# Optimization experiments

Measured on AMD Instinct MI355X. Metric: run time of the kernel, lower is better.

Reference implementation:

```python
import jax, jax.numpy as jnp
import numpy as np

ALPHA = 0.01
BETA = 3e-05
OUT_H, OUT_W = 256, 256
KSIZE, SIGMA = 5, 4.0


def _gaussian_kernel2d(ks=KSIZE, sigma=SIGMA):
    x = jnp.arange(ks, dtype=jnp.float32) - (ks - 1) / 2.0
    g = jnp.exp(-(x * x) / (2.0 * sigma * sigma))
    g = g / g.sum()
    return jnp.outer(g, g)  # [ks, ks]


def _gaussian_blur(maps):
    # maps: [B, H, W]; reflect padding + depthwise 5x5 gaussian (kornia-style GaussianBlur2d)
    k = _gaussian_kernel2d()[None, None]  # [1,1,5,5]
    p = KSIZE // 2
    x = jnp.pad(maps[:, None], ((0, 0), (0, 0), (p, p), (p, p)), mode='reflect')
    y = jax.lax.conv_general_dilated(x, k, (1, 1), 'VALID')
    return y[:, 0]


def _resize_bilinear_align_corners(x, oh, ow):
    # x: [B, h, w] -> [B, oh, ow], torch F.interpolate(mode='bilinear', align_corners=True)
    B, h, w = x.shape
    ys = jnp.linspace(0.0, h - 1.0, oh)
    xs = jnp.linspace(0.0, w - 1.0, ow)
    y0 = jnp.floor(ys).astype(jnp.int32)
    x0 = jnp.floor(xs).astype(jnp.int32)
    y1 = jnp.minimum(y0 + 1, h - 1)
    x1 = jnp.minimum(x0 + 1, w - 1)
    fy = (ys - y0.astype(ys.dtype))[:, None]  # [oh,1]
    fx = (xs - x0.astype(xs.dtype))[None, :]  # [1,ow]
    a = x[:, y0][:, :, x0]
    b = x[:, y0][:, :, x1]
    c = x[:, y1][:, :, x0]
    d = x[:, y1][:, :, x1]
    top = a * (1.0 - fx) + b * fx
    bot = c * (1.0 - fx) + d * fx
    return top * (1.0 - fy) + bot * fy


def setup_inputs() -> dict:
    key = jax.random.key(0)
    k0, k1, k2 = jax.random.split(key, 3)
    B = 256
    return {
        'out0': jax.random.normal(k0, (B, 64, 64), jnp.float32),
        'out1': jax.random.normal(k1, (B, 32, 32), jnp.float32),
        'out2': jax.random.normal(k2, (B, 16, 16), jnp.float32),
    }


def reference(out0, out1, out2):
    outputs = [out0, out1, out2]
    B = out0.shape[0]
    # per-sample max of each scale -> softmax-weighted selection of per-sample weight
    max_vals = jnp.stack([o.reshape(B, -1).max(axis=1) for o in outputs], axis=1)  # [B,3]
    probs = jax.nn.softmax(max_vals, axis=1)
    mask = probs > probs.mean(axis=1, keepdims=True)  # probs > prob_mean
    cnt = mask.sum(axis=1)
    sel_mean = (max_vals * mask).sum(axis=1) / jnp.maximum(cnt, 1)
    total_weights = jnp.where(cnt > 0, jnp.maximum(sel_mean * ALPHA, BETA), BETA)  # [B]
    # multi-scale fusion: bilinear(align_corners=True) upsample to (256,256) and sum
    maps = _resize_bilinear_align_corners(out0, OUT_H, OUT_W)
    maps = maps + _resize_bilinear_align_corners(out1, OUT_H, OUT_W)
    maps = maps + _resize_bilinear_align_corners(out2, OUT_H, OUT_W)
    # gaussian blur then per-sample score. torch takes topk(k=f(total_weights)).values[0],
    # and topk values are sorted descending, so values[0] == max (k / total_weights drop out).
    blurred = _gaussian_blur(maps)
    scores = blurred.reshape(B, -1).max(axis=1)
    del total_weights  # only influenced the (unused) top-k size in the original
    return scores[:, None], maps
```

## Files before the change

kernel.cpp:

```cpp
#include <hip/hip_runtime.h>
#include <math.h>


static constexpr int W  = 256;
static constexpr int QB = 16;

__device__ __forceinline__ int reflect256(int i) {
    if (i < 0) i = -i;
    if (i > 255) i = 510 - i;
    return i;
}

__global__ __launch_bounds__(256, 4) void fused_kernel(
    const float* __restrict__ in0,
    const float* __restrict__ in1,
    const float* __restrict__ in2,
    float* __restrict__ part,
    float* __restrict__ maps)
{
    const int t   = threadIdx.x;
    const int q   = t & 63;
    const int wv  = __builtin_amdgcn_readfirstlane(t >> 6);
    const int bid = blockIdx.x;
    const int b   = bid >> 4;
    const int r0  = (bid & 15) * 16;
    const int rw0 = r0 + wv * 4;
    const int c0  = q * 4;

    const int rlo = max(r0 - 2, 0);
    const int rhi = min(r0 + 17, 255);
    const int y0lo = (rlo * 63) / 255;
    const int y1lo = (rlo * 31) / 255;
    const int y2lo = (rlo * 15) / 255;
    const int y0hi = min((rhi * 63) / 255 + 1, 63);
    const int y1hi = min((rhi * 31) / 255 + 1, 31);
    const int y2hi = min((rhi * 15) / 255 + 1, 15);
    const int n0 = y0hi - y0lo + 1;
    const int n1 = y1hi - y1lo + 1;
    const int n2 = y2hi - y2lo + 1;

    __shared__ float lds[4768];
    float* const s0r = lds;
    float* const s1r = lds + 448;
    float* const s2r = lds + 608;
    float* const xr0 = lds + 672;
    float* const xr1 = lds + 2464;
    float* const xr2 = lds + 3744;

    {
        const float4* g0 = (const float4*)(in0 + (size_t)b * 4096 + y0lo * 64);
        const float4* g1 = (const float4*)(in1 + (size_t)b * 1024 + y1lo * 32);
        const float4* g2 = (const float4*)(in2 + (size_t)b * 256  + y2lo * 16);
        if (t < n0 * 16) ((float4*)s0r)[t] = g0[t];
        if (t < n1 * 8)  ((float4*)s1r)[t] = g1[t];
        if (t < n2 * 4)  ((float4*)s2r)[t] = g2[t];
    }
    __syncthreads();

    const float inv255 = 1.0f / 255.0f;

    {
        const int T0 = n0 * 64;
        for (int task = t; task < T0; task += 256) {
            const int r = task >> 6, cq = (task & 63) * 4;
            const float* src = s0r + r * 64;
            const int x0 = (cq * 63) / 255;
            const float v0 = src[x0];
            const float v1 = src[min(x0 + 1, 63)];
            const float v2 = src[min(x0 + 2, 63)];
            float o[4];
#pragma unroll
            for (int k = 0; k < 4; ++k) {
                const int ix = (cq + k) * 63;
                const int xk = ix / 255;
                const float fx = (float)(ix - 255 * xk) * inv255;
                const float a  = (xk == x0) ? v0 : v1;
                const float bb = (xk == x0) ? v1 : v2;
                o[k] = a + fx * (bb - a);
            }
            *(float4*)(xr0 + r * 256 + cq) = make_float4(o[0], o[1], o[2], o[3]);
        }
        const int T1 = n1 * 64;
        for (int task = t; task < T1; task += 256) {
            const int r = task >> 6, cq = (task & 63) * 4;
            const float* src = s1r + r * 32;
            const int x0 = (cq * 31) / 255;
            const float v0 = src[x0];
            const float v1 = src[min(x0 + 1, 31)];
            const float v2 = src[min(x0 + 2, 31)];
            float o[4];
#pragma unroll
            for (int k = 0; k < 4; ++k) {
                const int ix = (cq + k) * 31;
                const int xk = ix / 255;
                const float fx = (float)(ix - 255 * xk) * inv255;
                const float a  = (xk == x0) ? v0 : v1;
                const float bb = (xk == x0) ? v1 : v2;
                o[k] = a + fx * (bb - a);
            }
            *(float4*)(xr1 + r * 256 + cq) = make_float4(o[0], o[1], o[2], o[3]);
        }
        const int T2 = n2 * 64;
        for (int task = t; task < T2; task += 256) {
            const int r = task >> 6, cq = (task & 63) * 4;
            const float* src = s2r + r * 16;
            const int x0 = (cq * 15) / 255;
            const float v0 = src[x0];
            const float v1 = src[min(x0 + 1, 15)];
            const float v2 = src[min(x0 + 2, 15)];
            float o[4];
#pragma unroll
            for (int k = 0; k < 4; ++k) {
                const int ix = (cq + k) * 15;
                const int xk = ix / 255;
                const float fx = (float)(ix - 255 * xk) * inv255;
                const float a  = (xk == x0) ? v0 : v1;
                const float bb = (xk == x0) ? v1 : v2;
                o[k] = a + fx * (bb - a);
            }
            *(float4*)(xr2 + r * 256 + cq) = make_float4(o[0], o[1], o[2], o[3]);
        }
    }
    __syncthreads();

    auto ld0 = [&](int y, float* d) {
        const float4 v = *(const float4*)(xr0 + (y - y0lo) * 256 + c0);
        d[0] = v.x; d[1] = v.y; d[2] = v.z; d[3] = v.w;
    };
    auto ld1 = [&](int y, float* d) {
        const float4 v = *(const float4*)(xr1 + (y - y1lo) * 256 + c0);
        d[0] = v.x; d[1] = v.y; d[2] = v.z; d[3] = v.w;
    };
    auto ld2 = [&](int y, float* d) {
        const float4 v = *(const float4*)(xr2 + (y - y2lo) * 256 + c0);
        d[0] = v.x; d[1] = v.y; d[2] = v.z; d[3] = v.w;
    };

    int ya, yb, yc, rem0, rem1, rem2;
    float rl0[4], rh0[4], rl1[4], rh1[4], rl2[4], rh2[4];

    auto init_state = [&](int rn) {
        int iy;
        iy = rn * 63; ya = iy / 255; rem0 = iy - 255 * ya; ld0(ya, rl0); ld0(min(ya + 1, 63), rh0);
        iy = rn * 31; yb = iy / 255; rem1 = iy - 255 * yb; ld1(yb, rl1); ld1(min(yb + 1, 31), rh1);
        iy = rn * 15; yc = iy / 255; rem2 = iy - 255 * yc; ld2(yc, rl2); ld2(min(yc + 1, 15), rh2);
    };

    auto step = [&](float* o) {
        const float w0 = (float)rem0 * inv255;
        const float w1 = (float)rem1 * inv255;
        const float w2 = (float)rem2 * inv255;
#pragma unroll
        for (int k = 0; k < 4; ++k) {
            o[k] = (rl0[k] + w0 * (rh0[k] - rl0[k]))
                 + (rl1[k] + w1 * (rh1[k] - rl1[k]))
                 + (rl2[k] + w2 * (rh2[k] - rl2[k]));
        }
        rem0 += 63;
        if (rem0 >= 255) {
            rem0 -= 255; ++ya;
#pragma unroll
            for (int k = 0; k < 4; ++k) rl0[k] = rh0[k];
            ld0(min(ya + 1, 63), rh0);
        }
        rem1 += 31;
        if (rem1 >= 255) {
            rem1 -= 255; ++yb;
#pragma unroll
            for (int k = 0; k < 4; ++k) rl1[k] = rh1[k];
            ld1(min(yb + 1, 31), rh1);
        }
        rem2 += 15;
        if (rem2 >= 255) {
            rem2 -= 255; ++yc;
#pragma unroll
            for (int k = 0; k < 4; ++k) rl2[k] = rh2[k];
            ld2(min(yc + 1, 15), rh2);
        }
    };

    auto direct4 = [&](int rn, float* o) {
        const int ry = reflect256(rn);
        int iy = ry * 63; int a0 = iy / 255; float w0 = (float)(iy - 255 * a0) * inv255; int a1 = min(a0 + 1, 63);
        int ib = ry * 31; int b0 = ib / 255; float w1 = (float)(ib - 255 * b0) * inv255; int b1 = min(b0 + 1, 31);
        int ic = ry * 15; int cc0 = ic / 255; float w2 = (float)(ic - 255 * cc0) * inv255; int cc1 = min(cc0 + 1, 15);
        float l0[4], h0[4], l1[4], h1[4], l2[4], h2[4];
        ld0(a0, l0); ld0(a1, h0);
        ld1(b0, l1); ld1(b1, h1);
        ld2(cc0, l2); ld2(cc1, h2);
#pragma unroll
        for (int k = 0; k < 4; ++k) {
            o[k] = (l0[k] + w0 * (h0[k] - l0[k]))
                 + (l1[k] + w1 * (h1[k] - l1[k]))
                 + (l2[k] + w2 * (h2[k] - l2[k]));
        }
    };

    const float e1 = expf(-1.0f / 32.0f);
    const float e2 = expf(-4.0f / 32.0f);
    const float nrm = 1.0f + 2.0f * e1 + 2.0f * e2;
    const float gwc = 1.0f / nrm, gwa = e1 / nrm, gwb = e2 / nrm;

    float m0[4], m1[4], m2[4], m3[4], mn[4];
    if (rw0 == 0) {
        direct4(2, m0);
        direct4(1, m1);
        direct4(0, m2);
#pragma unroll
        for (int k = 0; k < 4; ++k) m3[k] = m1[k];
        init_state(2);
    } else {
        init_state(rw0 - 2);
        step(m0); step(m1); step(m2); step(m3);
    }

    float* __restrict__ mpr = maps + ((size_t)b * W + (size_t)rw0) * W + c0;
    *(float4*)(mpr)     = make_float4(m2[0], m2[1], m2[2], m2[3]);
    *(float4*)(mpr + W) = make_float4(m3[0], m3[1], m3[2], m3[3]);

    float gmax = -INFINITY;

#pragma unroll
    for (int i = 0; i < 4; ++i) {
        const int rn = rw0 + 2 + i;
        if (rn <= 255) step(mn);
        else           direct4(rn, mn);

        if (i < 2)
            *(float4*)(mpr + (size_t)(2 + i) * W) = make_float4(mn[0], mn[1], mn[2], mn[3]);

        float vr0 = gwb * (m0[0] + mn[0]) + gwa * (m1[0] + m3[0]) + gwc * m2[0];
        float vr1 = gwb * (m0[1] + mn[1]) + gwa * (m1[1] + m3[1]) + gwc * m2[1];
        float vr2 = gwb * (m0[2] + mn[2]) + gwa * (m1[2] + m3[2]) + gwc * m2[2];
        float vr3 = gwb * (m0[3] + mn[3]) + gwa * (m1[3] + m3[3]) + gwc * m2[3];
#pragma unroll
        for (int k = 0; k < 4; ++k) { m0[k] = m1[k]; m1[k] = m2[k]; m2[k] = m3[k]; m3[k] = mn[k]; }

        float az = __shfl_up(vr2, 1);
        float aw = __shfl_up(vr3, 1);
        float cx = __shfl_down(vr0, 1);
        float cy = __shfl_down(vr1, 1);
        float a2 = (q == 0)  ? vr2 : az;
        float a3 = (q == 0)  ? vr1 : aw;
        float c4 = (q == 63) ? vr2 : cx;
        float c5 = (q == 63) ? vr1 : cy;
        float o0 = gwc * vr0 + gwa * (a3 + vr1)  + gwb * (a2 + vr2);
        float o1 = gwc * vr1 + gwa * (vr0 + vr2) + gwb * (a3 + vr3);
        float o2 = gwc * vr2 + gwa * (vr1 + vr3) + gwb * (vr0 + c4);
        float o3 = gwc * vr3 + gwa * (vr2 + c4)  + gwb * (vr1 + c5);
        gmax = fmaxf(gmax, fmaxf(fmaxf(o0, o1), fmaxf(o2, o3)));
    }

#pragma unroll
    for (int off = 32; off > 0; off >>= 1)
        gmax = fmaxf(gmax, __shfl_down(gmax, off));
    if (q == 0) part[bid * 4 + wv] = gmax;
}

__global__ void reduce_kernel(const float* __restrict__ part,
                              float* __restrict__ scores, int B) {
    int i = blockIdx.x * blockDim.x + threadIdx.x;
    if (i < B) {
        const float4* p = (const float4*)(part + 64 * i);
        float m = -INFINITY;
#pragma unroll
        for (int k = 0; k < 16; ++k) {
            float4 v = p[k];
            m = fmaxf(m, fmaxf(fmaxf(v.x, v.y), fmaxf(v.z, v.w)));
        }
        scores[i] = m;
    }
}

extern "C" void kernel_launch(void* const* d_in, const int* in_sizes, int n_in,
                              void* d_out, int out_size, void* d_ws, size_t ws_size,
                              hipStream_t stream) {
    const float* in0 = (const float*)d_in[0];
    const float* in1 = (const float*)d_in[1];
    const float* in2 = (const float*)d_in[2];
    const int B = in_sizes[0] / (64 * 64);

    float* scores = (float*)d_out;
    float* maps   = (float*)d_out + B;
    float* part   = (float*)d_ws;

    hipLaunchKernelGGL(fused_kernel, dim3(B * QB), dim3(256), 0, stream,
                       in0, in1, in2, part, maps);
    hipLaunchKernelGGL(reduce_kernel, dim3((B + 255) / 256), dim3(256), 0, stream,
                       part, scores, B);
}
```

Baseline: 99.68 us.

## Double rows per block and interpolate the largest scale from raw rows

New measurement: 106.5 us. 1.07x slower.

```diff
diff --git a/kernel.cpp b/kernel.cpp
--- a/kernel.cpp
+++ b/kernel.cpp
@@ -3,7 +3,7 @@
 
 
 static constexpr int W  = 256;
-static constexpr int QB = 16;
+static constexpr int QB = 8;
 
 __device__ __forceinline__ int reflect256(int i) {
     if (i < 0) i = -i;
@@ -22,13 +22,13 @@
     const int q   = t & 63;
     const int wv  = __builtin_amdgcn_readfirstlane(t >> 6);
     const int bid = blockIdx.x;
-    const int b   = bid >> 4;
-    const int r0  = (bid & 15) * 16;
-    const int rw0 = r0 + wv * 4;
+    const int b   = bid >> 3;
+    const int r0  = (bid & 7) * 32;
+    const int rw0 = r0 + wv * 8;
     const int c0  = q * 4;
 
     const int rlo = max(r0 - 2, 0);
-    const int rhi = min(r0 + 17, 255);
+    const int rhi = min(r0 + 33, 255);
     const int y0lo = (rlo * 63) / 255;
     const int y1lo = (rlo * 31) / 255;
     const int y2lo = (rlo * 15) / 255;
@@ -39,13 +39,12 @@
     const int n1 = y1hi - y1lo + 1;
     const int n2 = y2hi - y2lo + 1;
 
-    __shared__ float lds[4768];
+    __shared__ float lds[4080];
     float* const s0r = lds;
-    float* const s1r = lds + 448;
-    float* const s2r = lds + 608;
-    float* const xr0 = lds + 672;
-    float* const xr1 = lds + 2464;
-    float* const xr2 = lds + 3744;
+    float* const s1r = lds + 704;
+    float* const s2r = lds + 928;
+    float* const xr1 = lds + 1008;
+    float* const xr2 = lds + 2800;
 
     {
         const float4* g0 = (const float4*)(in0 + (size_t)b * 4096 + y0lo * 64);
@@ -60,26 +59,6 @@
     const float inv255 = 1.0f / 255.0f;
 
     {
-        const int T0 = n0 * 64;
-        for (int task = t; task < T0; task += 256) {
-            const int r = task >> 6, cq = (task & 63) * 4;
-            const float* src = s0r + r * 64;
-            const int x0 = (cq * 63) / 255;
-            const float v0 = src[x0];
-            const float v1 = src[min(x0 + 1, 63)];
-            const float v2 = src[min(x0 + 2, 63)];
-            float o[4];
-#pragma unroll
-            for (int k = 0; k < 4; ++k) {
-                const int ix = (cq + k) * 63;
-                const int xk = ix / 255;
-                const float fx = (float)(ix - 255 * xk) * inv255;
-                const float a  = (xk == x0) ? v0 : v1;
-                const float bb = (xk == x0) ? v1 : v2;
-                o[k] = a + fx * (bb - a);
-            }
-            *(float4*)(xr0 + r * 256 + cq) = make_float4(o[0], o[1], o[2], o[3]);
-        }
         const int T1 = n1 * 64;
         for (int task = t; task < T1; task += 256) {
             const int r = task >> 6, cq = (task & 63) * 4;
@@ -123,9 +102,23 @@
     }
     __syncthreads();
 
-    auto ld0 = [&](int y, float* d) {
-        const float4 v = *(const float4*)(xr0 + (y - y0lo) * 256 + c0);
-        d[0] = v.x; d[1] = v.y; d[2] = v.z; d[3] = v.w;
+    int   x00[4];
+    float fx0[4];
+#pragma unroll
+    for (int k = 0; k < 4; ++k) {
+        int ix = (c0 + k) * 63;
+        x00[k] = ix / 255;
+        fx0[k] = (float)(ix - 255 * x00[k]) * inv255;
+    }
+
+    auto xg0 = [&](int y, float* d) {
+        const float* row = s0r + (y - y0lo) * 64;
+#pragma unroll
+        for (int k = 0; k < 4; ++k) {
+            const int xa = x00[k], xb = min(xa + 1, 63);
+            const float a = row[xa], bb = row[xb];
+            d[k] = a + fx0[k] * (bb - a);
+        }
     };
     auto ld1 = [&](int y, float* d) {
         const float4 v = *(const float4*)(xr1 + (y - y1lo) * 256 + c0);
@@ -141,7 +134,7 @@
 
     auto init_state = [&](int rn) {
         int iy;
-        iy = rn * 63; ya = iy / 255; rem0 = iy - 255 * ya; ld0(ya, rl0); ld0(min(ya + 1, 63), rh0);
+        iy = rn * 63; ya = iy / 255; rem0 = iy - 255 * ya; xg0(ya, rl0); xg0(min(ya + 1, 63), rh0);
         iy = rn * 31; yb = iy / 255; rem1 = iy - 255 * yb; ld1(yb, rl1); ld1(min(yb + 1, 31), rh1);
         iy = rn * 15; yc = iy / 255; rem2 = iy - 255 * yc; ld2(yc, rl2); ld2(min(yc + 1, 15), rh2);
     };
@@ -161,7 +154,7 @@
             rem0 -= 255; ++ya;
 #pragma unroll
             for (int k = 0; k < 4; ++k) rl0[k] = rh0[k];
-            ld0(min(ya + 1, 63), rh0);
+            xg0(min(ya + 1, 63), rh0);
         }
         rem1 += 31;
         if (rem1 >= 255) {
@@ -185,7 +178,7 @@
         int ib = ry * 31; int b0 = ib / 255; float w1 = (float)(ib - 255 * b0) * inv255; int b1 = min(b0 + 1, 31);
         int ic = ry * 15; int cc0 = ic / 255; float w2 = (float)(ic - 255 * cc0) * inv255; int cc1 = min(cc0 + 1, 15);
         float l0[4], h0[4], l1[4], h1[4], l2[4], h2[4];
-        ld0(a0, l0); ld0(a1, h0);
+        xg0(a0, l0); xg0(a1, h0);
         ld1(b0, l1); ld1(b1, h1);
         ld2(cc0, l2); ld2(cc1, h2);
 #pragma unroll
@@ -221,12 +214,12 @@
     float gmax = -INFINITY;
 
 #pragma unroll
-    for (int i = 0; i < 4; ++i) {
+    for (int i = 0; i < 8; ++i) {
         const int rn = rw0 + 2 + i;
         if (rn <= 255) step(mn);
         else           direct4(rn, mn);
 
-        if (i < 2)
+        if (i < 6)
             *(float4*)(mpr + (size_t)(2 + i) * W) = make_float4(mn[0], mn[1], mn[2], mn[3]);
 
         float vr0 = gwb * (m0[0] + mn[0]) + gwa * (m1[0] + m3[0]) + gwc * m2[0];
@@ -261,10 +254,10 @@
                               float* __restrict__ scores, int B) {
     int i = blockIdx.x * blockDim.x + threadIdx.x;
     if (i < B) {
-        const float4* p = (const float4*)(part + 64 * i);
+        const float4* p = (const float4*)(part + 32 * i);
         float m = -INFINITY;
 #pragma unroll
-        for (int k = 0; k < 16; ++k) {
+        for (int k = 0; k < 8; ++k) {
             float4 v = p[k];
             m = fmaxf(m, fmaxf(fmaxf(v.x, v.y), fmaxf(v.z, v.w)));
         }
```
